# Kernel optimization log

Hardware: AMD Instinct MI355X
Metric: run time of the kernel (lower is better)

The kernel has to match this reference:

```python
import jax, jax.numpy as jnp
import numpy as np

N_EDGES = 8192
TOTAL_TOKENS = 2097152
OUT_CH = 128


def setup_inputs() -> dict:
    key = jax.random.key(0)
    k1, k2, k3, k4, k5 = jax.random.split(key, 5)
    overlap_similarity = jax.random.uniform(k1, (N_EDGES,), dtype=jnp.float32)
    overlap_length = jax.random.normal(k2, (N_EDGES,), dtype=jnp.float32)
    # flattened DNA tokens (A,C,G,T -> 0..3) over all edges
    tokens = jax.random.randint(k3, (TOTAL_TOKENS,), 0, 4, dtype=jnp.int32)
    # sorted segment ids -> ragged variable-length reads per edge
    segment_ids = jnp.sort(jax.random.randint(k4, (TOTAL_TOKENS,), 0, N_EDGES, dtype=jnp.int32))
    embedding = jax.random.normal(k5, (4, OUT_CH), dtype=jnp.float32)
    return {
        "overlap_similarity": overlap_similarity,
        "overlap_length": overlap_length,
        "tokens": tokens,
        "segment_ids": segment_ids,
        "embedding": embedding,
        "n_edges": N_EDGES,
    }


def reference(overlap_similarity, overlap_length, tokens, segment_ids, embedding, n_edges):
    # Ragged embedding-bag mean: for each edge, mean of embedding[tokens] over its read.
    # (overlap_similarity / overlap_length are unused by the original forward's output.)
    embeds = embedding[tokens]  # [T, D]
    sums = jax.ops.segment_sum(embeds, segment_ids, num_segments=n_edges)  # [E, D]
    counts = jax.ops.segment_sum(
        jnp.ones((tokens.shape[0],), dtype=embeds.dtype), segment_ids, num_segments=n_edges
    )  # [E]
    return sums / jnp.maximum(counts, 1.0)[:, None]
```

## Files before the change

kernel.cpp:

```cpp
#include <hip/hip_runtime.h>

#define OUT_CH 128
#define WAVES_PER_BLOCK 4

__global__ void seg_starts_kernel(const int* __restrict__ segids,
                                  int* __restrict__ starts,
                                  int T, int E) {
    int i = blockIdx.x * blockDim.x + threadIdx.x;
    int k = i << 2;
    if (k >= T) return;
    const int4 s4 = *(const int4*)(segids + k);
    int s[5] = {s4.x, s4.y, s4.z, s4.w, 0};
    s[4] = (k + 4 < T) ? segids[k + 4] : E;
    if (k == 0) {
        for (int q = 0; q <= s4.x; ++q) starts[q] = 0;
    }
#pragma unroll
    for (int j = 0; j < 4; ++j) {
        for (int q = s[j] + 1; q <= s[j + 1]; ++q) starts[q] = k + j + 1;
    }
}

__global__ __launch_bounds__(WAVES_PER_BLOCK * 64)
void edge_out_kernel(const int* __restrict__ tokens,
                     const int* __restrict__ starts,
                     const float* __restrict__ emb,
                     float* __restrict__ out,
                     int E) {
    const int lane = threadIdx.x & 63;
    const int wid  = threadIdx.x >> 6;
    const int e = blockIdx.x * WAVES_PER_BLOCK + wid;
    if (e >= E) return;

    const int start = starts[e];
    const int end   = starts[e + 1];

    unsigned long long acc = 0;
    for (int k = start + lane; k < end; k += 64) {
        acc += 1ull << (tokens[k] << 4);
    }
#pragma unroll
    for (int m = 32; m > 0; m >>= 1) {
        acc += __shfl_xor(acc, m, 64);
    }

    const float c0 = (float)(acc & 0xFFFFull);
    const float c1 = (float)((acc >> 16) & 0xFFFFull);
    const float c2 = (float)((acc >> 32) & 0xFFFFull);
    const float c3 = (float)((acc >> 48) & 0xFFFFull);
    const float tot = c0 + c1 + c2 + c3;
    const float inv = 1.0f / fmaxf(tot, 1.0f);

    const int c = lane << 1;
    const float2 e0 = *(const float2*)(emb + 0 * OUT_CH + c);
    const float2 e1 = *(const float2*)(emb + 1 * OUT_CH + c);
    const float2 e2 = *(const float2*)(emb + 2 * OUT_CH + c);
    const float2 e3 = *(const float2*)(emb + 3 * OUT_CH + c);

    float2 r;
    r.x = (c0 * e0.x + c1 * e1.x + c2 * e2.x + c3 * e3.x) * inv;
    r.y = (c0 * e0.y + c1 * e1.y + c2 * e2.y + c3 * e3.y) * inv;
    *(float2*)(out + (size_t)e * OUT_CH + c) = r;
}

extern "C" void kernel_launch(void* const* d_in, const int* in_sizes, int n_in,
                              void* d_out, int out_size, void* d_ws, size_t ws_size,
                              hipStream_t stream) {
    const int* tokens = (const int*)d_in[2];
    const int* segids = (const int*)d_in[3];
    const float* emb  = (const float*)d_in[4];
    float* out = (float*)d_out;

    const int T = in_sizes[2];
    const int E = out_size / OUT_CH;

    int* starts = (int*)d_ws;

    const int threadsA = (T + 3) / 4;
    const int blocksA = (threadsA + 255) / 256;
    seg_starts_kernel<<<blocksA, 256, 0, stream>>>(segids, starts, T, E);

    const int blocksB = (E + WAVES_PER_BLOCK - 1) / WAVES_PER_BLOCK;
    edge_out_kernel<<<blocksB, WAVES_PER_BLOCK * 64, 0, stream>>>(
        tokens, starts, emb, out, E);
}
```

Measured before the change: 81.61 us.

## Fuse segment-start computation into edge kernel via per-wave 32-ary search

Drops the separate kernel that scanned all segment ids to build a starts array. Each wave now finds its own segment bounds with a 32-way parallel search over the sorted segment ids: half the wave searches for the start, half for the end. Token reads are widened to int4 loads with boundary masking. This removes a full pass over the segment-id array and one kernel launch, at the cost of a few dependent global-load rounds per wave.

```diff
diff --git a/kernel.cpp b/kernel.cpp
--- a/kernel.cpp
+++ b/kernel.cpp
@@ -3,41 +3,52 @@
 #define OUT_CH 128
 #define WAVES_PER_BLOCK 4
 
-__global__ void seg_starts_kernel(const int* __restrict__ segids,
-                                  int* __restrict__ starts,
-                                  int T, int E) {
-    int i = blockIdx.x * blockDim.x + threadIdx.x;
-    int k = i << 2;
-    if (k >= T) return;
-    const int4 s4 = *(const int4*)(segids + k);
-    int s[5] = {s4.x, s4.y, s4.z, s4.w, 0};
-    s[4] = (k + 4 < T) ? segids[k + 4] : E;
-    if (k == 0) {
-        for (int q = 0; q <= s4.x; ++q) starts[q] = 0;
-    }
-#pragma unroll
-    for (int j = 0; j < 4; ++j) {
-        for (int q = s[j] + 1; q <= s[j + 1]; ++q) starts[q] = k + j + 1;
-    }
-}
-
 __global__ __launch_bounds__(WAVES_PER_BLOCK * 64)
-void edge_out_kernel(const int* __restrict__ tokens,
-                     const int* __restrict__ starts,
-                     const float* __restrict__ emb,
-                     float* __restrict__ out,
-                     int E) {
+void edge_fused_kernel(const int* __restrict__ tokens,
+                       const int* __restrict__ segids,
+                       const float* __restrict__ emb,
+                       float* __restrict__ out,
+                       int T, int E) {
     const int lane = threadIdx.x & 63;
     const int wid  = threadIdx.x >> 6;
     const int e = blockIdx.x * WAVES_PER_BLOCK + wid;
     if (e >= E) return;
 
-    const int start = starts[e];
-    const int end   = starts[e + 1];
+    const int grp    = lane >> 5;
+    const int sub    = lane & 31;
+    const int target = e + grp;
+
+    int lo = 0, hi = T;
+    while (hi > lo) {
+        const int len = hi - lo;
+        const int pos = lo + (((sub + 1) * len) >> 5);
+        const bool c = (pos >= T) || (segids[pos] >= target);
+        const unsigned long long bal = __ballot(c);
+        const unsigned int gm = (unsigned int)(bal >> (grp << 5));
+        const int f = __ffs(gm) - 1;
+        const int nhi = lo + (((f + 1) * len) >> 5);
+        const int nlo = (f == 0) ? lo : (lo + ((f * len) >> 5) + 1);
+        hi = nhi;
+        lo = nlo;
+    }
+    const int start = __shfl(lo, 0, 64);
+    const int end   = __shfl(lo, 32, 64);
 
     unsigned long long acc = 0;
-    for (int k = start + lane; k < end; k += 64) {
-        acc += 1ull << (tokens[k] << 4);
+    const int base = start & ~3;
+    for (int k = base + (lane << 2); k < end; k += WAVES_PER_BLOCK * 64) {
+        const int4 t4 = *(const int4*)(tokens + k);
+        if (k >= start && k + 3 < end) {
+            acc += 1ull << (t4.x << 4);
+            acc += 1ull << (t4.y << 4);
+            acc += 1ull << (t4.z << 4);
+            acc += 1ull << (t4.w << 4);
+        } else {
+            if (k + 0 >= start && k + 0 < end) acc += 1ull << (t4.x << 4);
+            if (k + 1 >= start && k + 1 < end) acc += 1ull << (t4.y << 4);
+            if (k + 2 >= start && k + 2 < end) acc += 1ull << (t4.z << 4);
+            if (k + 3 >= start && k + 3 < end) acc += 1ull << (t4.w << 4);
+        }
     }
 #pragma unroll
     for (int m = 32; m > 0; m >>= 1) {
@@ -74,13 +85,7 @@
     const int T = in_sizes[2];
     const int E = out_size / OUT_CH;
 
-    int* starts = (int*)d_ws;
-
-    const int threadsA = (T + 3) / 4;
-    const int blocksA = (threadsA + 255) / 256;
-    seg_starts_kernel<<<blocksA, 256, 0, stream>>>(segids, starts, T, E);
-
-    const int blocksB = (E + WAVES_PER_BLOCK - 1) / WAVES_PER_BLOCK;
-    edge_out_kernel<<<blocksB, WAVES_PER_BLOCK * 64, 0, stream>>>(
-        tokens, starts, emb, out, E);
+    const int blocks = (E + WAVES_PER_BLOCK - 1) / WAVES_PER_BLOCK;
+    edge_fused_kernel<<<blocks, WAVES_PER_BLOCK * 64, 0, stream>>>(
+        tokens, segids, emb, out, T, E);
 }
```

Result: no change. 83.14 us (+1.9%).
